# Kernel optimization log

Measured on AMD Instinct MI355X. Metric: run time of the kernel, lower is better.

## Reference

```python
import jax, jax.numpy as jnp
import numpy as np
from jax import lax

BATCH = 8192
PATCH = 2
STRIDE = 2
OUT_CH = 4
NUM_PATCHES = ((28 - PATCH) // STRIDE + 1) ** 2  # 196
THRESHOLD = 0.8
EPS = 1e-12


def setup_inputs() -> dict:
    key = jax.random.key(0)
    k1, k2, k3, k4, k5 = jax.random.split(key, 5)
    x = jax.random.normal(k1, (BATCH, 1, 28, 28), dtype=jnp.float32)
    conv_w = jax.random.normal(k2, (OUT_CH, 1, PATCH, PATCH), dtype=jnp.float32) * 0.5
    conv_b = jax.random.normal(k3, (OUT_CH,), dtype=jnp.float32) * 0.1
    feat_dim = OUT_CH * NUM_PATCHES + NUM_PATCHES  # 784 + 196 = 980
    lin_w = jax.random.normal(k4, (10, feat_dim), dtype=jnp.float32) * 0.02
    lin_b = jax.random.normal(k5, (10,), dtype=jnp.float32) * 0.01
    return {"x": x, "conv_w": conv_w, "conv_b": conv_b, "lin_w": lin_w, "lin_b": lin_b}


def reference(x, conv_w, conv_b, lin_w, lin_b):
    # conv patch embed: (B,1,28,28) -> (B,C,14,14)
    f = lax.conv_general_dilated(
        x, conv_w, window_strides=(STRIDE, STRIDE), padding="VALID",
        dimension_numbers=("NCHW", "OIHW", "NCHW"))
    f = f + conv_b[None, :, None, None]
    B = f.shape[0]
    flat = f.reshape(B, -1)  # (B, C*P) channel-major, matches torch .view
    # replicate feat.view(num_patches, -1): rows of length C from the flat vector
    pf = flat.reshape(B, NUM_PATCHES, -1)  # (B, P, C)
    nrm = pf / (jnp.linalg.norm(pf, axis=-1, keepdims=True) + EPS)
    # squared cosine similarity = state fidelity, all pairs at once
    fid = jnp.einsum("bpc,bqc->bpq", nrm, nrm) ** 2  # (B, P, P)
    w = (fid >= THRESHOLD).astype(flat.dtype)
    w = w * (1.0 - jnp.eye(NUM_PATCHES, dtype=flat.dtype))  # no self-edges
    deg = jnp.sum(w, axis=-1)  # weighted degree per node, (B, P)
    feats = jnp.concatenate([flat, deg], axis=1)  # (B, 980)
    logits = feats @ lin_w.T + lin_b
    return jax.nn.log_softmax(logits, axis=-1)
```

## Files before the change

### kernel.cpp

```cpp
#include <hip/hip_runtime.h>
#include <math.h>


#define NP 196
#define FEAT 980
#define COS_TH 0.894427190999915878f

typedef short v4s  __attribute__((ext_vector_type(4)));
typedef short v8s  __attribute__((ext_vector_type(8)));
typedef float v16f __attribute__((ext_vector_type(16)));

static __device__ __forceinline__ float bf2f(short s) {
    return __uint_as_float(((uint32_t)(uint16_t)s) << 16);
}

__global__ __launch_bounds__(256, 6) void quanv_kernel(
    const float* __restrict__ x,
    const float* __restrict__ conv_w,
    const float* __restrict__ conv_b,
    const float* __restrict__ lin_w,
    const float* __restrict__ lin_b,
    float* __restrict__ out)
{
    __shared__ __align__(16) float s_x[2][784];
    __shared__ __align__(16) short s_P[2][256][8];
    __shared__ __align__(16) float s_feats[2][FEAT];

    int*   s_deg    = (int*)s_x;
    int*   s_cred   = s_deg + 384;
    float* s_part   = (float*)(s_cred + 392);
    float* s_logits = s_part + 500;

    const int b = blockIdx.x;
    const int t = threadIdx.x;
    const int w = t >> 6, l = t & 63;

    if (t < NP) {
        ((float4*)s_x[0])[t] = ((const float4*)(x + (size_t)(2 * b)     * 784))[t];
        ((float4*)s_x[1])[t] = ((const float4*)(x + (size_t)(2 * b + 1) * 784))[t];
    }
    __syncthreads();

    if (t < NP) {
        int h = t / 14, ww = t - 14 * (t / 14);
        #pragma unroll
        for (int img = 0; img < 2; ++img) {
            const float* r0 = s_x[img] + (2 * h) * 28 + 2 * ww;
            float x00 = r0[0], x01 = r0[1], x10 = r0[28], x11 = r0[29];
            #pragma unroll
            for (int c = 0; c < 4; ++c) {
                float f = conv_b[c]
                        + conv_w[c * 4 + 0] * x00 + conv_w[c * 4 + 1] * x01
                        + conv_w[c * 4 + 2] * x10 + conv_w[c * 4 + 3] * x11;
                s_feats[img][c * NP + t] = f;
            }
        }
    }
    __syncthreads();

    {
        #pragma unroll
        for (int img = 0; img < 2; ++img) {
            v8s pk = {0, 0, 0, 0, 0, 0, 0, 0};
            if (t < NP) {
                float4 v = ((const float4*)s_feats[img])[t];
                float n = sqrtf(v.x * v.x + v.y * v.y + v.z * v.z + v.w * v.w);
                float inv = 1.0f / (n + 1e-12f);
                float e[4] = { v.x * inv, v.y * inv, v.z * inv, v.w * inv };
                #pragma unroll
                for (int k = 0; k < 4; ++k) {
                    uint32_t bx = __float_as_uint(e[k]);
                    uint32_t rh = bx + 0x7FFFu + ((bx >> 16) & 1u);
                    uint32_t hk = rh >> 16;
                    float hif = __uint_as_float(hk << 16);
                    float res = e[k] - hif;
                    uint32_t br = __float_as_uint(res);
                    uint32_t rl = br + 0x7FFFu + ((br >> 16) & 1u);
                    pk[k]     = (short)hk;
                    pk[4 + k] = (short)(rl >> 16);
                }
            }
            *(v8s*)&s_P[img][t][0] = pk;
        }
        if (t < NP) { s_cred[t] = 0; s_cred[196 + t] = 0; }
    }
    __syncthreads();

    v16f zacc = {0.f,0.f,0.f,0.f,0.f,0.f,0.f,0.f,
                 0.f,0.f,0.f,0.f,0.f,0.f,0.f,0.f};
    asm("" : "+v"(zacc));

    const int ln = l & 31, half = l >> 5;

    #pragma unroll
    for (int jj = 0; jj < 3; ++jj) {
        const int job = w + 4 * jj;
        const int img = (job >= 6) ? 1 : 0;
        const int j = job - 6 * img;
        const short* Pbase = &s_P[img][0][0];

        v4s bh = *(const v4s*)(Pbase + (32 * j + ln) * 8 + 4 * half);
        v8s B = __builtin_shufflevector(bh, bh, 0, 1, 2, 3, 0, 1, 2, 3);

        unsigned c0 = 0u, c1 = 0u;
        #pragma unroll
        for (int i = 0; i < 6; ++i) {
            v8s A = *(const v8s*)(Pbase + (32 * i + ln) * 8);
            v16f acc = __builtin_amdgcn_mfma_f32_32x32x16_bf16(A, B, zacc, 0, 0, 0);
            #pragma unroll
            for (int e = 0; e < 16; e += 2) {
                c0 += (fabsf(acc[e])     >= COS_TH) ? 1u : 0u;
                c1 += (fabsf(acc[e + 1]) >= COS_TH) ? 1u : 0u;
            }
        }
        unsigned cnt = c0 + c1;
        cnt += __shfl_down(cnt, 32, 64);
        if (l < 32)
            s_deg[img * 192 + 32 * j + l] = (int)cnt;
    }

    #pragma unroll
    for (int img = 0; img < 2; ++img) {
        const int r = 192 + w;
        const short* pr = &s_P[img][r][0];
        float pe0 = bf2f(pr[0]) + bf2f(pr[4]);
        float pe1 = bf2f(pr[1]) + bf2f(pr[5]);
        float pe2 = bf2f(pr[2]) + bf2f(pr[6]);
        float pe3 = bf2f(pr[3]) + bf2f(pr[7]);
        unsigned total = 0u;
        #pragma unroll
        for (int k = 0; k < 4; ++k) {
            int q = 64 * k + l;
            const short* qr = &s_P[img][q][0];
            float d =          pe0 * (bf2f(qr[0]) + bf2f(qr[4]));
            d = fmaf(pe1, bf2f(qr[1]) + bf2f(qr[5]), d);
            d = fmaf(pe2, bf2f(qr[2]) + bf2f(qr[6]), d);
            d = fmaf(pe3, bf2f(qr[3]) + bf2f(qr[7]), d);
            bool hit = fabsf(d) >= COS_TH;
            unsigned long long m = __ballot(hit);
            total += (unsigned)__popcll(m);
            if (hit && q < 192)
                atomicAdd(&s_cred[img * 196 + q], 1);
        }
        if (l == 0)
            s_feats[img][784 + r] = (float)(int)total - 1.0f;
    }
    __syncthreads();

    if (t < 192) {
        s_feats[0][784 + t] = (float)(s_deg[t]       + s_cred[t])       - 1.0f;
        s_feats[1][784 + t] = (float)(s_deg[192 + t] + s_cred[196 + t]) - 1.0f;
    }
    __syncthreads();

    if (t < 250) {
        int k = t / 25, c = t - 25 * (t / 25);
        const float4* wrow = (const float4*)(lin_w + k * FEAT);
        const float4* f0p = (const float4*)s_feats[0];
        const float4* f1p = (const float4*)s_feats[1];
        float a0 = 0.0f, a1 = 0.0f;
        for (int i = c; i < 245; i += 25) {
            float4 wv = wrow[i];
            float4 f0 = f0p[i];
            float4 f1 = f1p[i];
            a0 = fmaf(f0.x, wv.x, a0); a1 = fmaf(f1.x, wv.x, a1);
            a0 = fmaf(f0.y, wv.y, a0); a1 = fmaf(f1.y, wv.y, a1);
            a0 = fmaf(f0.z, wv.z, a0); a1 = fmaf(f1.z, wv.z, a1);
            a0 = fmaf(f0.w, wv.w, a0); a1 = fmaf(f1.w, wv.w, a1);
        }
        s_part[t]       = a0;
        s_part[250 + t] = a1;
    }
    __syncthreads();

    if (t < 20) {
        int img = t / 10, k = t - 10 * (t / 10);
        const float* part = s_part + 250 * img;
        float s = lin_b[k];
        #pragma unroll
        for (int i = 0; i < 25; ++i) s += part[k * 25 + i];
        s_logits[10 * img + k] = s;
    }
    __syncthreads();

    if (t < 20) {
        int img = t / 10, k = t - 10 * (t / 10);
        const float* lg = s_logits + 10 * img;
        float m = -INFINITY;
        #pragma unroll
        for (int j2 = 0; j2 < 10; ++j2) m = fmaxf(m, lg[j2]);
        float s = 0.0f;
        #pragma unroll
        for (int j2 = 0; j2 < 10; ++j2) s += expf(lg[j2] - m);
        out[(size_t)(2 * b + img) * 10 + k] = lg[k] - m - logf(s);
    }
}

extern "C" void kernel_launch(void* const* d_in, const int* in_sizes, int n_in,
                              void* d_out, int out_size, void* d_ws, size_t ws_size,
                              hipStream_t stream) {
    const float* x      = (const float*)d_in[0];
    const float* conv_w = (const float*)d_in[1];
    const float* conv_b = (const float*)d_in[2];
    const float* lin_w  = (const float*)d_in[3];
    const float* lin_b  = (const float*)d_in[4];
    float* out = (float*)d_out;
    quanv_kernel<<<dim3(4096), dim3(256), 0, stream>>>(x, conv_w, conv_b, lin_w, lin_b, out);
}
```

Baseline: 104.4 us.

## Process four images per block and load conv inputs directly from global

Each 256-thread block now handles four images instead of two, halving the grid and amortizing the lin_w row reads and the block-level fixed costs across more images. The staging copy of x into shared memory and its barrier are removed; each thread instead reads its 2x2 patch straight from global memory as two float2 loads. Shared memory per block grows and the occupancy hint drops from 6 to 4 blocks per CU, so there is less latency hiding and longer serial MFMA and tail work per block.

Result: slower. 107.0 us (+2.5%).

```diff
diff --git a/kernel.cpp b/kernel.cpp
--- a/kernel.cpp
+++ b/kernel.cpp
@@ -14,7 +14,7 @@
     return __uint_as_float(((uint32_t)(uint16_t)s) << 16);
 }
 
-__global__ __launch_bounds__(256, 6) void quanv_kernel(
+__global__ __launch_bounds__(256, 4) void quanv_kernel(
     const float* __restrict__ x,
     const float* __restrict__ conv_w,
     const float* __restrict__ conv_b,
@@ -22,36 +22,29 @@
     const float* __restrict__ lin_b,
     float* __restrict__ out)
 {
-    __shared__ __align__(16) float s_x[2][784];
-    __shared__ __align__(16) short s_P[2][256][8];
-    __shared__ __align__(16) float s_feats[2][FEAT];
-
-    int*   s_deg    = (int*)s_x;
-    int*   s_cred   = s_deg + 384;
-    float* s_part   = (float*)(s_cred + 392);
-    float* s_logits = s_part + 500;
+    __shared__ __align__(16) short s_P[4][256][8];
+    __shared__ __align__(16) float s_feats[4][FEAT];
+    __shared__ int s_deg[4][192];
+    __shared__ int s_cred[4][196];
+    float* s_part   = (float*)s_P;
+    float* s_logits = (float*)s_P + 1000;
 
     const int b = blockIdx.x;
     const int t = threadIdx.x;
     const int w = t >> 6, l = t & 63;
 
     if (t < NP) {
-        ((float4*)s_x[0])[t] = ((const float4*)(x + (size_t)(2 * b)     * 784))[t];
-        ((float4*)s_x[1])[t] = ((const float4*)(x + (size_t)(2 * b + 1) * 784))[t];
-    }
-    __syncthreads();
-
-    if (t < NP) {
         int h = t / 14, ww = t - 14 * (t / 14);
         #pragma unroll
-        for (int img = 0; img < 2; ++img) {
-            const float* r0 = s_x[img] + (2 * h) * 28 + 2 * ww;
-            float x00 = r0[0], x01 = r0[1], x10 = r0[28], x11 = r0[29];
+        for (int img = 0; img < 4; ++img) {
+            const float* ib = x + (size_t)(4 * b + img) * 784 + 56 * h + 2 * ww;
+            float2 r0 = *(const float2*)(ib);
+            float2 r1 = *(const float2*)(ib + 28);
             #pragma unroll
             for (int c = 0; c < 4; ++c) {
                 float f = conv_b[c]
-                        + conv_w[c * 4 + 0] * x00 + conv_w[c * 4 + 1] * x01
-                        + conv_w[c * 4 + 2] * x10 + conv_w[c * 4 + 3] * x11;
+                        + conv_w[c * 4 + 0] * r0.x + conv_w[c * 4 + 1] * r0.y
+                        + conv_w[c * 4 + 2] * r1.x + conv_w[c * 4 + 3] * r1.y;
                 s_feats[img][c * NP + t] = f;
             }
         }
@@ -60,7 +53,7 @@
 
     {
         #pragma unroll
-        for (int img = 0; img < 2; ++img) {
+        for (int img = 0; img < 4; ++img) {
             v8s pk = {0, 0, 0, 0, 0, 0, 0, 0};
             if (t < NP) {
                 float4 v = ((const float4*)s_feats[img])[t];
@@ -82,7 +75,10 @@
             }
             *(v8s*)&s_P[img][t][0] = pk;
         }
-        if (t < NP) { s_cred[t] = 0; s_cred[196 + t] = 0; }
+        if (t < NP) {
+            s_cred[0][t] = 0; s_cred[1][t] = 0;
+            s_cred[2][t] = 0; s_cred[3][t] = 0;
+        }
     }
     __syncthreads();
 
@@ -93,9 +89,9 @@
     const int ln = l & 31, half = l >> 5;
 
     #pragma unroll
-    for (int jj = 0; jj < 3; ++jj) {
+    for (int jj = 0; jj < 6; ++jj) {
         const int job = w + 4 * jj;
-        const int img = (job >= 6) ? 1 : 0;
+        const int img = job / 6;
         const int j = job - 6 * img;
         const short* Pbase = &s_P[img][0][0];
 
@@ -116,11 +112,11 @@
         unsigned cnt = c0 + c1;
         cnt += __shfl_down(cnt, 32, 64);
         if (l < 32)
-            s_deg[img * 192 + 32 * j + l] = (int)cnt;
+            s_deg[img][32 * j + l] = (int)cnt;
     }
 
     #pragma unroll
-    for (int img = 0; img < 2; ++img) {
+    for (int img = 0; img < 4; ++img) {
         const int r = 192 + w;
         const short* pr = &s_P[img][r][0];
         float pe0 = bf2f(pr[0]) + bf2f(pr[4]);
@@ -140,7 +136,7 @@
             unsigned long long m = __ballot(hit);
             total += (unsigned)__popcll(m);
             if (hit && q < 192)
-                atomicAdd(&s_cred[img * 196 + q], 1);
+                atomicAdd(&s_cred[img][q], 1);
         }
         if (l == 0)
             s_feats[img][784 + r] = (float)(int)total - 1.0f;
@@ -148,8 +144,9 @@
     __syncthreads();
 
     if (t < 192) {
-        s_feats[0][784 + t] = (float)(s_deg[t]       + s_cred[t])       - 1.0f;
-        s_feats[1][784 + t] = (float)(s_deg[192 + t] + s_cred[196 + t]) - 1.0f;
+        #pragma unroll
+        for (int img = 0; img < 4; ++img)
+            s_feats[img][784 + t] = (float)(s_deg[img][t] + s_cred[img][t]) - 1.0f;
     }
     __syncthreads();
 
@@ -158,22 +155,29 @@
         const float4* wrow = (const float4*)(lin_w + k * FEAT);
         const float4* f0p = (const float4*)s_feats[0];
         const float4* f1p = (const float4*)s_feats[1];
-        float a0 = 0.0f, a1 = 0.0f;
+        const float4* f2p = (const float4*)s_feats[2];
+        const float4* f3p = (const float4*)s_feats[3];
+        float a0 = 0.f, a1 = 0.f, a2 = 0.f, a3 = 0.f;
         for (int i = c; i < 245; i += 25) {
             float4 wv = wrow[i];
-            float4 f0 = f0p[i];
-            float4 f1 = f1p[i];
-            a0 = fmaf(f0.x, wv.x, a0); a1 = fmaf(f1.x, wv.x, a1);
-            a0 = fmaf(f0.y, wv.y, a0); a1 = fmaf(f1.y, wv.y, a1);
-            a0 = fmaf(f0.z, wv.z, a0); a1 = fmaf(f1.z, wv.z, a1);
-            a0 = fmaf(f0.w, wv.w, a0); a1 = fmaf(f1.w, wv.w, a1);
+            float4 v0 = f0p[i], v1 = f1p[i], v2 = f2p[i], v3 = f3p[i];
+            a0 = fmaf(v0.x, wv.x, a0); a1 = fmaf(v1.x, wv.x, a1);
+            a2 = fmaf(v2.x, wv.x, a2); a3 = fmaf(v3.x, wv.x, a3);
+            a0 = fmaf(v0.y, wv.y, a0); a1 = fmaf(v1.y, wv.y, a1);
+            a2 = fmaf(v2.y, wv.y, a2); a3 = fmaf(v3.y, wv.y, a3);
+            a0 = fmaf(v0.z, wv.z, a0); a1 = fmaf(v1.z, wv.z, a1);
+            a2 = fmaf(v2.z, wv.z, a2); a3 = fmaf(v3.z, wv.z, a3);
+            a0 = fmaf(v0.w, wv.w, a0); a1 = fmaf(v1.w, wv.w, a1);
+            a2 = fmaf(v2.w, wv.w, a2); a3 = fmaf(v3.w, wv.w, a3);
         }
         s_part[t]       = a0;
         s_part[250 + t] = a1;
-    }
-    __syncthreads();
-
-    if (t < 20) {
+        s_part[500 + t] = a2;
+        s_part[750 + t] = a3;
+    }
+    __syncthreads();
+
+    if (t < 40) {
         int img = t / 10, k = t - 10 * (t / 10);
         const float* part = s_part + 250 * img;
         float s = lin_b[k];
@@ -183,7 +187,7 @@
     }
     __syncthreads();
 
-    if (t < 20) {
+    if (t < 40) {
         int img = t / 10, k = t - 10 * (t / 10);
         const float* lg = s_logits + 10 * img;
         float m = -INFINITY;
@@ -192,7 +196,7 @@
         float s = 0.0f;
         #pragma unroll
         for (int j2 = 0; j2 < 10; ++j2) s += expf(lg[j2] - m);
-        out[(size_t)(2 * b + img) * 10 + k] = lg[k] - m - logf(s);
+        out[(size_t)(4 * b + img) * 10 + k] = lg[k] - m - logf(s);
     }
 }
 
@@ -205,5 +209,5 @@
     const float* lin_w  = (const float*)d_in[3];
     const float* lin_b  = (const float*)d_in[4];
     float* out = (float*)d_out;
-    quanv_kernel<<<dim3(4096), dim3(256), 0, stream>>>(x, conv_w, conv_b, lin_w, lin_b, out);
+    quanv_kernel<<<dim3(2048), dim3(256), 0, stream>>>(x, conv_w, conv_b, lin_w, lin_b, out);
 }
```
